# Kernel tuning notes

Hardware: AMD Instinct MI355X
Metric: run time of the kernel (lower is better)

## Reference

```python
import jax, jax.numpy as jnp
import numpy as np

VOCAB = 333
D_MODEL = 333
N_HEADS = 8
D_HEAD = 64
INNER = N_HEADS * D_HEAD  # 512
MAX_LEN = 333
B, S = 64, 333


def setup_inputs() -> dict:
    key = jax.random.key(0)
    ks = jax.random.split(key, 9)
    sc_in = (1.0 / np.sqrt(D_MODEL)).astype(np.float32)
    sc_inner = (1.0 / np.sqrt(INNER)).astype(np.float32)
    return {
        "xs": jax.random.randint(ks[0], (B, S), 0, VOCAB),
        "emb": jax.random.normal(ks[1], (VOCAB, D_MODEL), dtype=jnp.float32),
        "Wq": jax.random.normal(ks[2], (D_MODEL, INNER), dtype=jnp.float32) * sc_in,
        "bq": jnp.zeros((INNER,), dtype=jnp.float32),
        "Wk": jax.random.normal(ks[3], (D_MODEL, INNER), dtype=jnp.float32) * sc_in,
        "bk": jnp.zeros((INNER,), dtype=jnp.float32),
        "Wv": jax.random.normal(ks[4], (D_MODEL, INNER), dtype=jnp.float32) * sc_in,
        "bv": jnp.zeros((INNER,), dtype=jnp.float32),
        "Er": jax.random.normal(ks[5], (MAX_LEN, D_HEAD), dtype=jnp.float32) * 0.02,
        "Wo": jax.random.normal(ks[6], (INNER, D_MODEL), dtype=jnp.float32) * sc_inner,
        "bo": jnp.zeros((D_MODEL,), dtype=jnp.float32),
    }


def _skew(qe):
    # Music Transformer skew trick: qe [B,H,S,L] (L==S) -> Srel [B,H,S,S]
    b, h, s, l = qe.shape
    padded = jnp.pad(qe, ((0, 0), (0, 0), (0, 0), (1, 0)))  # [B,H,S,L+1]
    return padded.reshape(b, h, l + 1, s)[:, :, 1:, :]       # [B,H,S,S]


def reference(xs, emb, Wq, bq, Wk, bk, Wv, bv, Er, Wo, bo):
    x = emb[xs]  # [B,S,D]
    b, s, _ = x.shape

    def heads(w, bias):
        return (x @ w + bias).reshape(b, s, N_HEADS, D_HEAD).transpose(0, 2, 1, 3)

    q = heads(Wq, bq)  # [B,H,S,Dh]
    k = heads(Wk, bk)
    v = heads(Wv, bv)

    er = Er[MAX_LEN - s:]                                   # [S,Dh]
    qk = jnp.einsum("bhsd,bhtd->bhst", q, k)               # content scores
    srel = _skew(jnp.einsum("bhsd,ld->bhsl", q, er))       # relative scores
    scores = (qk + srel) / np.sqrt(D_HEAD).astype(np.float32)

    causal = jnp.tril(jnp.ones((s, s), dtype=bool))         # predictive mask
    scores = jnp.where(causal, scores, jnp.float32(-1e9))
    attn = jax.nn.softmax(scores, axis=-1)

    out = jnp.einsum("bhst,bhtd->bhsd", attn, v)            # [B,H,S,Dh]
    out = out.transpose(0, 2, 1, 3).reshape(b, s, INNER)
    return out @ Wo + bo                                    # [B,S,D]
```

## Files before the change

kernel.cpp:

```cpp
#include <hip/hip_runtime.h>
#include <hip/hip_bf16.h>

#define BB 64
#define SS 333
#define NH 8
#define DH 64
#define NI 512
#define DM 333
#define M1 21312
#define KP 384
#define NQ 1536
#define RS1 1536
#define VT2 110889

typedef __attribute__((ext_vector_type(8))) short short8v;
typedef __attribute__((ext_vector_type(4))) float f32x4;

__device__ inline short f2bf(float f) {
    unsigned u = __float_as_uint(f);
    u += 0x7fffu + ((u >> 16) & 1u);
    return (short)(u >> 16);
}

__device__ __forceinline__ void gload16(const void* g, void* l) {
    __builtin_amdgcn_global_load_lds(
        (const __attribute__((address_space(1))) void*)g,
        (__attribute__((address_space(3))) void*)l, 16, 0, 0);
}

#define CN0 (SS * DH)
#define CN1 (DM * KP)
#define CN2 (NQ * KP)
#define CN3 (384 * NI)
#define CNT (CN0 + CN1 + CN2 + CN3)

__global__ __launch_bounds__(256) void conv_all_kernel(
    const float* __restrict__ Er, const float* __restrict__ emb,
    const float* __restrict__ Wq, const float* __restrict__ Wk,
    const float* __restrict__ Wv, const float* __restrict__ Wo,
    short* __restrict__ eb, short* __restrict__ embb,
    short* __restrict__ wt, short* __restrict__ wot)
{
    int i = blockIdx.x * 256 + threadIdx.x;
    if (i < CN0) {
        eb[i] = f2bf(Er[i]);
        return;
    }
    i -= CN0;
    if (i < CN1) {
        int v = i / KP, k = i - v * KP;
        embb[i] = (k < DM) ? f2bf(emb[(size_t)v * DM + k]) : (short)0;
        return;
    }
    i -= CN1;
    if (i < CN2) {
        int n = i / KP, k = i - n * KP;
        int mat = n >> 9, c = n & 511;
        const float* W = (mat == 0) ? Wq : (mat == 1) ? Wk : Wv;
        wt[i] = (k < DM) ? f2bf(W[(size_t)k * NI + c]) : (short)0;
        return;
    }
    i -= CN2;
    if (i < CN3) {
        int n = i >> 9, k = i & 511;
        wot[i] = (n < DM) ? f2bf(Wo[(size_t)k * DM + n]) : (short)0;
    }
}

__global__ __launch_bounds__(256) void yqkv_kernel(
    const short* __restrict__ embb, const short* __restrict__ wt,
    const float* __restrict__ bq, const float* __restrict__ bk, const float* __restrict__ bv,
    short* __restrict__ Y)
{
    __shared__ __align__(16) short abuf[2][128 * 64];
    __shared__ __align__(16) short bbuf[2][128 * 64];

    const int row0 = blockIdx.x * 128;
    const int n0   = blockIdx.y * 128;
    const int t = threadIdx.x;
    const int lane = t & 63, w = t >> 6;
    const int l15 = lane & 15, lq = lane >> 4;
    const int wr = w >> 1, wc = w & 1;

    f32x4 acc[4][4];
#pragma unroll
    for (int mi = 0; mi < 4; ++mi)
#pragma unroll
        for (int nj = 0; nj < 4; ++nj) { f32x4 z = {0.f,0.f,0.f,0.f}; acc[mi][nj] = z; }

    auto stage = [&](int buf, int k0) {
#pragma unroll
        for (int i = 0; i < 4; ++i) {
            int idx = (w * 4 + i) * 64 + lane;
            int row = idx >> 3, sp = idx & 7;
            int ar = row0 + row; ar = ar < DM ? ar : DM - 1;
            gload16(embb + (size_t)ar * KP + k0 + ((sp ^ (row & 7)) << 3),
                    &abuf[buf][(w * 4 + i) * 512]);
        }
#pragma unroll
        for (int i = 0; i < 4; ++i) {
            int idx = (w * 4 + i) * 64 + lane;
            int row = idx >> 3, sp = idx & 7;
            gload16(wt + (size_t)(n0 + row) * KP + k0 + ((sp ^ (row & 7)) << 3),
                    &bbuf[buf][(w * 4 + i) * 512]);
        }
    };

    stage(0, 0);
    __syncthreads();
    for (int tk = 0; tk < 6; ++tk) {
        if (tk < 5) stage((tk + 1) & 1, (tk + 1) * 64);
        const short* ab = abuf[tk & 1];
        const short* bb = bbuf[tk & 1];
#pragma unroll
        for (int kh = 0; kh < 2; ++kh) {
            short8v af[4], bfv[4];
#pragma unroll
            for (int mi = 0; mi < 4; ++mi) {
                int row = wr * 64 + mi * 16 + l15;
                int sp = (lq + 4 * kh) ^ (row & 7);
                af[mi] = *(const short8v*)(ab + row * 64 + sp * 8);
            }
#pragma unroll
            for (int nj = 0; nj < 4; ++nj) {
                int row = wc * 64 + nj * 16 + l15;
                int sp = (lq + 4 * kh) ^ (row & 7);
                bfv[nj] = *(const short8v*)(bb + row * 64 + sp * 8);
            }
            __builtin_amdgcn_s_setprio(1);
#pragma unroll
            for (int mi = 0; mi < 4; ++mi)
#pragma unroll
                for (int nj = 0; nj < 4; ++nj)
                    acc[mi][nj] = __builtin_amdgcn_mfma_f32_16x16x32_bf16(af[mi], bfv[nj], acc[mi][nj], 0, 0, 0);
            __builtin_amdgcn_s_setprio(0);
        }
        __syncthreads();
    }

    const int mat = n0 >> 9;
    const float* bias = (mat == 0) ? bq : (mat == 1) ? bk : bv;
    const int cb = (n0 & 511) + wc * 64;
#pragma unroll
    for (int nj = 0; nj < 4; ++nj) {
        float bvv = bias[cb + nj * 16 + l15];
        int colg = n0 + wc * 64 + nj * 16 + l15;
#pragma unroll
        for (int mi = 0; mi < 4; ++mi)
#pragma unroll
            for (int r = 0; r < 4; ++r) {
                int rowg = row0 + wr * 64 + mi * 16 + lq * 4 + r;
                Y[(size_t)rowg * NQ + colg] = f2bf(acc[mi][nj][r] + bvv);
            }
    }
}

__global__ __launch_bounds__(256) void qet_kernel(
    const short* __restrict__ Y, const short* __restrict__ eb,
    float* __restrict__ QEt)
{
    __shared__ __align__(16) short abuf[128 * 64];
    __shared__ __align__(16) short bbuf[128 * 64];

    const int row0 = blockIdx.x * 128;
    const int n0   = blockIdx.y * 128;
    const int h    = blockIdx.z;
    const int t = threadIdx.x;
    const int lane = t & 63, w = t >> 6;
    const int l15 = lane & 15, lq = lane >> 4;
    const int wr = w >> 1, wc = w & 1;

#pragma unroll
    for (int i = 0; i < 4; ++i) {
        int idx = (w * 4 + i) * 64 + lane;
        int row = idx >> 3, sp = idx & 7;
        int ar = row0 + row; ar = ar < DM ? ar : DM - 1;
        gload16(Y + (size_t)ar * RS1 + h * 64 + ((sp ^ (row & 7)) << 3),
                &abuf[(w * 4 + i) * 512]);
    }
#pragma unroll
    for (int i = 0; i < 4; ++i) {
        int idx = (w * 4 + i) * 64 + lane;
        int row = idx >> 3, sp = idx & 7;
        int br = n0 + row; br = br < SS ? br : SS - 1;
        gload16(eb + (size_t)br * DH + ((sp ^ (row & 7)) << 3),
                &bbuf[(w * 4 + i) * 512]);
    }
    __syncthreads();

    f32x4 acc[4][4];
#pragma unroll
    for (int mi = 0; mi < 4; ++mi)
#pragma unroll
        for (int nj = 0; nj < 4; ++nj) { f32x4 z = {0.f,0.f,0.f,0.f}; acc[mi][nj] = z; }

#pragma unroll
    for (int kh = 0; kh < 2; ++kh) {
        short8v af[4], bfv[4];
#pragma unroll
        for (int mi = 0; mi < 4; ++mi) {
            int row = wr * 64 + mi * 16 + l15;
            int sp = (lq + 4 * kh) ^ (row & 7);
            af[mi] = *(const short8v*)(abuf + row * 64 + sp * 8);
        }
#pragma unroll
        for (int nj = 0; nj < 4; ++nj) {
            int row = wc * 64 + nj * 16 + l15;
            int sp = (lq + 4 * kh) ^ (row & 7);
            bfv[nj] = *(const short8v*)(bbuf + row * 64 + sp * 8);
        }
#pragma unroll
        for (int mi = 0; mi < 4; ++mi)
#pragma unroll
            for (int nj = 0; nj < 4; ++nj)
                acc[mi][nj] = __builtin_amdgcn_mfma_f32_16x16x32_bf16(af[mi], bfv[nj], acc[mi][nj], 0, 0, 0);
    }

    float* Qh = QEt + (size_t)h * VT2;
#pragma unroll
    for (int nj = 0; nj < 4; ++nj) {
        int colg = n0 + wc * 64 + nj * 16 + l15;
#pragma unroll
        for (int mi = 0; mi < 4; ++mi)
#pragma unroll
            for (int r = 0; r < 4; ++r) {
                int rowg = row0 + wr * 64 + mi * 16 + lq * 4 + r;
                if (rowg < SS && colg < SS)
                    Qh[(size_t)rowg * SS + colg] = acc[mi][nj][r] * 0.125f - 16.0f;
            }
    }
}

__global__ __launch_bounds__(512) __attribute__((amdgpu_waves_per_eu(4, 4)))
void attn_mfma_kernel(
    const short* __restrict__ Y, const int* __restrict__ xs,
    const float* __restrict__ QEt, short* __restrict__ attnb)
{
    __shared__ __align__(16) short k_lds[64 * 64];
    __shared__ __align__(16) short vT_lds[64 * 64];
    __shared__ __align__(16) short vrow[64 * 64];
    __shared__ __align__(16) short p_lds[128 * 64];
    __shared__ int tok_lds[SS];

    const int p = blockIdx.x;
    const int h = p & 7;
    const int rem = p >> 3;
    const int pi = rem % 3;
    const int b = rem / 3;
    const int t = threadIdx.x;
    const int lane = t & 63, w = t >> 6;
    const int l15 = lane & 15, lq = lane >> 4;

    if (t < SS) tok_lds[t] = xs[b * SS + t];
    __syncthreads();

    const int thi = 5 - pi;
    const int tlo = pi;
    const int tt = w >> 2;
    const int sw = w & 3;
    const int ti = tt ? tlo : thi;
    const int iw = ti * 64 + 16 * sw;

    const short* Yh = Y + h * 64;
    const float* QEh = QEt + (size_t)h * VT2;

    int qr = iw + l15; if (qr > SS - 1) qr = SS - 1;
    const short* qrow = Yh + (size_t)tok_lds[qr] * RS1;
    const short8v qa0 = *(const short8v*)(qrow + lq * 8);
    const short8v qa1 = *(const short8v*)(qrow + 32 + lq * 8);

    int irow[4];
#pragma unroll
    for (int r = 0; r < 4; ++r) {
        int i_ = iw + lq * 4 + r; if (i_ > SS - 1) i_ = SS - 1;
        irow[r] = tok_lds[i_] * SS;
    }

    float l4[4];
    f32x4 o[4];
#pragma unroll
    for (int r = 0; r < 4; ++r) { l4[r] = 0.f; }
#pragma unroll
    for (int nd = 0; nd < 4; ++nd) { f32x4 z = {0.f, 0.f, 0.f, 0.f}; o[nd] = z; }

    asm volatile("s_waitcnt vmcnt(0)" ::: "memory");

    const int maxjs = thi;
    for (int js = 0; js <= maxjs; ++js) {
        const int j0 = js * 64;
        __syncthreads();
        {
            int row = t >> 3, sp = t & 7;
            int jg = j0 + row; if (jg > SS - 1) jg = SS - 1;
            gload16(Yh + (size_t)tok_lds[jg] * RS1 + 1024 + ((sp ^ (row & 7)) << 3),
                    &vrow[(size_t)(t & 448) * 8]);
        }
        {
            int row = t >> 3, sp = t & 7;
            int jg = j0 + row; if (jg > SS - 1) jg = SS - 1;
            gload16(Yh + (size_t)tok_lds[jg] * RS1 + 512 + ((sp ^ (row & 7)) << 3),
                    &k_lds[(size_t)(t & 448) * 8]);
        }
        asm volatile("s_waitcnt vmcnt(1)" ::: "memory");
        {
            const int kc = w;
            const int d = lane;
            short8v vv;
#pragma unroll
            for (int j = 0; j < 8; ++j)
                vv[j] = vrow[(kc * 8 + j) * 64 + (((d >> 3) ^ j) << 3) + (d & 7)];
            *(short8v*)(vT_lds + (size_t)d * 64 + ((kc ^ (d & 7)) << 3)) = vv;
        }
        __syncthreads();

        if (tt == 0 || js <= tlo) {
            f32x4 sc[4];
            __builtin_amdgcn_s_setprio(1);
#pragma unroll
            for (int n = 0; n < 4; ++n) {
                int row = n * 16 + l15;
                short8v k0 = *(const short8v*)((char*)k_lds + ((row * 128 + lq * 16) ^ ((row & 7) << 4)));
                short8v k1 = *(const short8v*)((char*)k_lds + ((row * 128 + 64 + lq * 16) ^ ((row & 7) << 4)));
                f32x4 z = {0.f, 0.f, 0.f, 0.f};
                z = __builtin_amdgcn_mfma_f32_16x16x32_bf16(qa0, k0, z, 0, 0, 0);
                sc[n] = __builtin_amdgcn_mfma_f32_16x16x32_bf16(qa1, k1, z, 0, 0, 0);
            }
            __builtin_amdgcn_s_setprio(0);

            short* pw = p_lds + w * 1024;
#pragma unroll
            for (int n = 0; n < 4; ++n) {
                float psum[4];
#pragma unroll
                for (int r = 0; r < 4; ++r) {
                    int irel = lq * 4 + r;
                    int li = (SS - 1) - (iw + irel) + j0 + n * 16 + l15;
                    li = li < 0 ? 0 : (li > SS - 1 ? SS - 1 : li);
                    float qet = QEh[irow[r] + li];
                    int jrel = n * 16 + l15;
                    bool ok = (j0 + jrel) <= (iw + irel);
                    float pv = ok ? __expf(sc[n][r] * 0.125f + qet) : 0.f;
                    psum[r] = pv;
                    *(short*)((char*)pw + ((irel * 128 + jrel * 2) ^ ((irel & 7) << 4))) = f2bf(pv);
                }
#pragma unroll
                for (int r = 0; r < 4; ++r)
                    l4[r] += psum[r];
            }

            __builtin_amdgcn_s_setprio(1);
#pragma unroll
            for (int kb2 = 0; kb2 < 2; ++kb2) {
                short8v pa = *(const short8v*)((char*)pw + ((l15 * 128 + kb2 * 64 + lq * 16) ^ ((l15 & 7) << 4)));
#pragma unroll
                for (int nd = 0; nd < 4; ++nd) {
                    int d = nd * 16 + l15;
                    short8v vf = *(const short8v*)((char*)vT_lds + ((size_t)d * 128 + (((kb2 * 4 + lq) ^ (d & 7)) << 4)));
                    o[nd] = __builtin_amdgcn_mfma_f32_16x16x32_bf16(pa, vf, o[nd], 0, 0, 0);
                }
            }
            __builtin_amdgcn_s_setprio(0);
        }
    }

#pragma unroll
    for (int r = 0; r < 4; ++r) {
        float ls = l4[r];
        ls += __shfl_xor(ls, 1);
        ls += __shfl_xor(ls, 2);
        ls += __shfl_xor(ls, 4);
        ls += __shfl_xor(ls, 8);
        int i = iw + lq * 4 + r;
        if (i < SS) {
            float rl = 1.0f / ls;
#pragma unroll
            for (int nd = 0; nd < 4; ++nd)
                attnb[(size_t)(b * SS + i) * NI + h * 64 + nd * 16 + l15] = f2bf(o[nd][r] * rl);
        }
    }
}

__global__ __launch_bounds__(256) void oproj_mfma_kernel(
    const short* __restrict__ ab_g, const short* __restrict__ wot,
    const float* __restrict__ bo, float* __restrict__ out)
{
    __shared__ __align__(16) short abuf[2][128 * 64];
    __shared__ __align__(16) short bbuf[2][128 * 64];

    const int row0 = blockIdx.x * 128;
    const int n0   = blockIdx.y * 128;
    const int t = threadIdx.x;
    const int lane = t & 63, w = t >> 6;
    const int l15 = lane & 15, lq = lane >> 4;
    const int wr = w >> 1, wc = w & 1;

    f32x4 acc[4][4];
#pragma unroll
    for (int mi = 0; mi < 4; ++mi)
#pragma unroll
        for (int nj = 0; nj < 4; ++nj) { f32x4 z = {0.f,0.f,0.f,0.f}; acc[mi][nj] = z; }

    auto stage = [&](int buf, int k0) {
#pragma unroll
        for (int i = 0; i < 4; ++i) {
            int idx = (w * 4 + i) * 64 + lane;
            int row = idx >> 3, sp = idx & 7;
            int rg = row0 + row; rg = rg < M1 ? rg : M1 - 1;
            gload16(ab_g + (size_t)rg * NI + k0 + ((sp ^ (row & 7)) << 3),
                    &abuf[buf][(w * 4 + i) * 512]);
        }
#pragma unroll
        for (int i = 0; i < 4; ++i) {
            int idx = (w * 4 + i) * 64 + lane;
            int row = idx >> 3, sp = idx & 7;
            gload16(wot + (size_t)(n0 + row) * NI + k0 + ((sp ^ (row & 7)) << 3),
                    &bbuf[buf][(w * 4 + i) * 512]);
        }
    };

    stage(0, 0);
    __syncthreads();
    for (int tk = 0; tk < 8; ++tk) {
        if (tk < 7) stage((tk + 1) & 1, (tk + 1) * 64);
        const short* ab = abuf[tk & 1];
        const short* bb = bbuf[tk & 1];
#pragma unroll
        for (int kh = 0; kh < 2; ++kh) {
            short8v af[4], bfv[4];
#pragma unroll
            for (int mi = 0; mi < 4; ++mi) {
                int row = wr * 64 + mi * 16 + l15;
                int sp = (lq + 4 * kh) ^ (row & 7);
                af[mi] = *(const short8v*)(ab + row * 64 + sp * 8);
            }
#pragma unroll
            for (int nj = 0; nj < 4; ++nj) {
                int row = wc * 64 + nj * 16 + l15;
                int sp = (lq + 4 * kh) ^ (row & 7);
                bfv[nj] = *(const short8v*)(bb + row * 64 + sp * 8);
            }
            __builtin_amdgcn_s_setprio(1);
#pragma unroll
            for (int mi = 0; mi < 4; ++mi)
#pragma unroll
                for (int nj = 0; nj < 4; ++nj)
                    acc[mi][nj] = __builtin_amdgcn_mfma_f32_16x16x32_bf16(af[mi], bfv[nj], acc[mi][nj], 0, 0, 0);
            __builtin_amdgcn_s_setprio(0);
        }
        __syncthreads();
    }

#pragma unroll
    for (int nj = 0; nj < 4; ++nj) {
        int colg = n0 + wc * 64 + nj * 16 + l15;
        float bvv = (colg < DM) ? bo[colg] : 0.f;
#pragma unroll
        for (int mi = 0; mi < 4; ++mi)
#pragma unroll
            for (int r = 0; r < 4; ++r) {
                int rowg = row0 + wr * 64 + mi * 16 + lq * 4 + r;
                if (rowg < M1 && colg < DM)
                    out[(size_t)rowg * DM + colg] = acc[mi][nj][r] + bvv;
            }
    }
}

extern "C" void kernel_launch(void* const* d_in, const int* in_sizes, int n_in,
                              void* d_out, int out_size, void* d_ws, size_t ws_size,
                              hipStream_t stream) {
    const int*   xs  = (const int*)d_in[0];
    const float* emb = (const float*)d_in[1];
    const float* Wq  = (const float*)d_in[2];
    const float* bq  = (const float*)d_in[3];
    const float* Wk  = (const float*)d_in[4];
    const float* bk  = (const float*)d_in[5];
    const float* Wv  = (const float*)d_in[6];
    const float* bv  = (const float*)d_in[7];
    const float* Er  = (const float*)d_in[8];
    const float* Wo  = (const float*)d_in[9];
    const float* bo  = (const float*)d_in[10];
    float* out = (float*)d_out;

    short* attnb = (short*)d_ws;
    short* Y    = attnb + (size_t)M1 * NI;
    short* embb = Y + (size_t)384 * NQ;
    short* wt   = embb + (size_t)DM * KP;
    short* wot  = wt + (size_t)NQ * KP;
    short* eb   = wot + (size_t)384 * NI;
    float* QEt  = (float*)(eb + (size_t)SS * DH);

    conv_all_kernel<<<(CNT + 255) / 256, 256, 0, stream>>>(Er, emb, Wq, Wk, Wv, Wo,
                                                           eb, embb, wt, wot);
    dim3 g1(3, 12);
    yqkv_kernel<<<g1, 256, 0, stream>>>(embb, wt, bq, bk, bv, Y);
    dim3 g2(3, 3, 8);
    qet_kernel<<<g2, 256, 0, stream>>>(Y, eb, QEt);
    attn_mfma_kernel<<<BB * NH * 3, 512, 0, stream>>>(Y, xs, QEt, attnb);
    dim3 g3((M1 + 127) / 128, 3);
    oproj_mfma_kernel<<<g3, 256, 0, stream>>>(attnb, wot, bo, out);
}
```

Measured before the change: 112.8 us.

## Pair two batches per block sharing query tile instead of causal tile pairing

```diff
diff --git a/kernel.cpp b/kernel.cpp
--- a/kernel.cpp
+++ b/kernel.cpp
@@ -236,36 +236,37 @@
     const short* __restrict__ Y, const int* __restrict__ xs,
     const float* __restrict__ QEt, short* __restrict__ attnb)
 {
-    __shared__ __align__(16) short k_lds[64 * 64];
-    __shared__ __align__(16) short vT_lds[64 * 64];
-    __shared__ __align__(16) short vrow[64 * 64];
+    __shared__ __align__(16) short k_lds[2][64 * 64];
+    __shared__ __align__(16) short vT_lds[2][64 * 64];
+    __shared__ __align__(16) short vrow[2][64 * 64];
     __shared__ __align__(16) short p_lds[128 * 64];
-    __shared__ int tok_lds[SS];
+    __shared__ int tok_lds[2][SS];
 
     const int p = blockIdx.x;
     const int h = p & 7;
     const int rem = p >> 3;
-    const int pi = rem % 3;
-    const int b = rem / 3;
+    const int tid = rem >> 5;
+    const int bp  = rem & 31;
+    const int ti  = 5 - tid;
     const int t = threadIdx.x;
     const int lane = t & 63, w = t >> 6;
     const int l15 = lane & 15, lq = lane >> 4;
-
-    if (t < SS) tok_lds[t] = xs[b * SS + t];
+    const int g  = w >> 2;
+    const int wl = w & 3;
+    const int b  = bp * 2 + g;
+    const int iw = ti * 64 + 16 * wl;
+    const int tl = t & 255;
+
+    for (int idx = t; idx < SS; idx += 512) tok_lds[0][idx] = xs[(bp * 2) * SS + idx];
+    for (int idx = t; idx < SS; idx += 512) tok_lds[1][idx] = xs[(bp * 2 + 1) * SS + idx];
     __syncthreads();
-
-    const int thi = 5 - pi;
-    const int tlo = pi;
-    const int tt = w >> 2;
-    const int sw = w & 3;
-    const int ti = tt ? tlo : thi;
-    const int iw = ti * 64 + 16 * sw;
 
     const short* Yh = Y + h * 64;
     const float* QEh = QEt + (size_t)h * VT2;
+    const int* tok = tok_lds[g];
 
     int qr = iw + l15; if (qr > SS - 1) qr = SS - 1;
-    const short* qrow = Yh + (size_t)tok_lds[qr] * RS1;
+    const short* qrow = Yh + (size_t)tok[qr] * RS1;
     const short8v qa0 = *(const short8v*)(qrow + lq * 8);
     const short8v qa1 = *(const short8v*)(qrow + 32 + lq * 8);
 
@@ -273,7 +274,7 @@
 #pragma unroll
     for (int r = 0; r < 4; ++r) {
         int i_ = iw + lq * 4 + r; if (i_ > SS - 1) i_ = SS - 1;
-        irow[r] = tok_lds[i_] * SS;
+        irow[r] = tok[i_] * SS;
     }
 
     float l4[4];
@@ -285,42 +286,47 @@
 
     asm volatile("s_waitcnt vmcnt(0)" ::: "memory");
 
-    const int maxjs = thi;
-    for (int js = 0; js <= maxjs; ++js) {
+    for (int js = 0; js <= ti; ++js) {
         const int j0 = js * 64;
         __syncthreads();
-        {
-            int row = t >> 3, sp = t & 7;
+#pragma unroll
+        for (int it = 0; it < 2; ++it) {
+            int task = it * 256 + tl;
+            int row = task >> 3, sp = task & 7;
             int jg = j0 + row; if (jg > SS - 1) jg = SS - 1;
-            gload16(Yh + (size_t)tok_lds[jg] * RS1 + 1024 + ((sp ^ (row & 7)) << 3),
-                    &vrow[(size_t)(t & 448) * 8]);
-        }
-        {
-            int row = t >> 3, sp = t & 7;
+            gload16(Yh + (size_t)tok[jg] * RS1 + 1024 + ((sp ^ (row & 7)) << 3),
+                    &vrow[g][(size_t)(it * 256 + (tl & 192)) * 8]);
+        }
+#pragma unroll
+        for (int it = 0; it < 2; ++it) {
+            int task = it * 256 + tl;
+            int row = task >> 3, sp = task & 7;
             int jg = j0 + row; if (jg > SS - 1) jg = SS - 1;
-            gload16(Yh + (size_t)tok_lds[jg] * RS1 + 512 + ((sp ^ (row & 7)) << 3),
-                    &k_lds[(size_t)(t & 448) * 8]);
-        }
-        asm volatile("s_waitcnt vmcnt(1)" ::: "memory");
-        {
-            const int kc = w;
+            gload16(Yh + (size_t)tok[jg] * RS1 + 512 + ((sp ^ (row & 7)) << 3),
+                    &k_lds[g][(size_t)(it * 256 + (tl & 192)) * 8]);
+        }
+        asm volatile("s_waitcnt vmcnt(2)" ::: "memory");
+#pragma unroll
+        for (int it = 0; it < 2; ++it) {
+            const int kc = it * 4 + wl;
             const int d = lane;
             short8v vv;
 #pragma unroll
             for (int j = 0; j < 8; ++j)
-                vv[j] = vrow[(kc * 8 + j) * 64 + (((d >> 3) ^ j) << 3) + (d & 7)];
-            *(short8v*)(vT_lds + (size_t)d * 64 + ((kc ^ (d & 7)) << 3)) = vv;
+                vv[j] = vrow[g][(kc * 8 + j) * 64 + (((d >> 3) ^ j) << 3) + (d & 7)];
+            *(short8v*)(vT_lds[g] + (size_t)d * 64 + ((kc ^ (d & 7)) << 3)) = vv;
         }
         __syncthreads();
 
-        if (tt == 0 || js <= tlo) {
+        {
+            const short* kb = k_lds[g];
             f32x4 sc[4];
             __builtin_amdgcn_s_setprio(1);
 #pragma unroll
             for (int n = 0; n < 4; ++n) {
                 int row = n * 16 + l15;
-                short8v k0 = *(const short8v*)((char*)k_lds + ((row * 128 + lq * 16) ^ ((row & 7) << 4)));
-                short8v k1 = *(const short8v*)((char*)k_lds + ((row * 128 + 64 + lq * 16) ^ ((row & 7) << 4)));
+                short8v k0 = *(const short8v*)((char*)kb + ((row * 128 + lq * 16) ^ ((row & 7) << 4)));
+                short8v k1 = *(const short8v*)((char*)kb + ((row * 128 + 64 + lq * 16) ^ ((row & 7) << 4)));
                 f32x4 z = {0.f, 0.f, 0.f, 0.f};
                 z = __builtin_amdgcn_mfma_f32_16x16x32_bf16(qa0, k0, z, 0, 0, 0);
                 sc[n] = __builtin_amdgcn_mfma_f32_16x16x32_bf16(qa1, k1, z, 0, 0, 0);
@@ -355,7 +361,7 @@
 #pragma unroll
                 for (int nd = 0; nd < 4; ++nd) {
                     int d = nd * 16 + l15;
-                    short8v vf = *(const short8v*)((char*)vT_lds + ((size_t)d * 128 + (((kb2 * 4 + lq) ^ (d & 7)) << 4)));
+                    short8v vf = *(const short8v*)((char*)vT_lds[g] + ((size_t)d * 128 + (((kb2 * 4 + lq) ^ (d & 7)) << 4)));
                     o[nd] = __builtin_amdgcn_mfma_f32_16x16x32_bf16(pa, vf, o[nd], 0, 0, 0);
                 }
             }
```

Result: faster. 104.7 us, median of 2 (-7.1%).
